# Optimization experiments

Measured on AMD Instinct MI355X. Metric: run time of the kernel, lower is better.

The kernel has to match this reference:

```python
import jax, jax.numpy as jnp
import numpy as np

BS, MA, H, NH = 64, 64, 64, 4  # molecules, max atoms per molecule, hsize, n_heads


def _lengths():
    # deterministic ragged molecule sizes in [24, 64]
    return np.array([24 + (7 * i) % 41 for i in range(BS)], dtype=np.int64)


def _scopes():
    lengths = _lengths()
    N = int(lengths.sum())  # 2774
    scope = np.zeros((BS, MA), dtype=np.int64)      # pad slots gather row 0 (zeros)
    rev = np.zeros((N,), dtype=np.int64)            # flat atom -> b*MA + slot
    pos = 1                                          # flat row 0 is the zero pad row
    for b, L in enumerate(lengths):
        scope[b, :L] = np.arange(pos, pos + L)
        rev[pos - 1:pos - 1 + L] = b * MA + np.arange(L)
        pos += L
    return scope, rev, N


def setup_inputs() -> dict:
    key = jax.random.key(0)
    k0, k1, k2, k3 = jax.random.split(key, 4)
    scope, rev, N = _scopes()
    inputs = jax.random.normal(k0, (N + 1, H), dtype=jnp.float32)
    inputs = inputs.at[0].set(0.0)  # zero pad row, as in graphretro flat tensors
    Wa_pair = jax.random.normal(k1, (H, H * NH), dtype=jnp.float32) * (1.0 / np.sqrt(H))
    Wa_score = jax.random.normal(k2, (H, NH), dtype=jnp.float32) * (1.0 / np.sqrt(H))
    W_proj = jax.random.normal(k3, (H * NH, H), dtype=jnp.float32) * (1.0 / np.sqrt(H * NH))
    return {
        "inputs": inputs,
        "scope_tensor": jnp.asarray(scope),
        "scope_rev_tensor": jnp.asarray(rev),
        "Wa_pair": Wa_pair,
        "Wa_score": Wa_score,
        "W_proj": W_proj,
    }


def reference(inputs, scope_tensor, scope_rev_tensor, Wa_pair, Wa_score, W_proj):
    bs, ma = scope_tensor.shape
    h = inputs.shape[1]
    nh = Wa_score.shape[1]
    # flat_to_batch: [bs, ma, h]; pad slots pull the zero row 0
    c_batch = inputs[scope_tensor]
    # get_pair: pairwise sum of atom embeddings -> [bs, ma, ma, h]
    atom_pair = c_batch[:, :, None, :] + c_batch[:, None, :, :]
    # Wa_pair (no bias) + relu, viewed as [bs, ma, ma, h, nh]
    total_att = jax.nn.relu(atom_pair @ Wa_pair).reshape(bs, ma, ma, h, nh)
    # einsum '...hn,hjn->...jn' with j==1, then sigmoid -> [bs, ma, ma, nh]
    att_score = jax.nn.sigmoid(jnp.einsum('bijhn,hn->bijn', total_att, Wa_score))
    # att_score * c_atom[b,j,h], summed over j -> [bs, ma, h, nh]
    c_sum = jnp.einsum('bijn,bjh->bihn', att_score, c_batch)
    # view to [bs, ma, h*nh] (h-major, matching torch .view) and project
    c_atom_att = c_sum.reshape(bs, ma, h * nh) @ W_proj  # [bs, ma, h]
    c_mol_att = c_atom_att.sum(axis=1)  # [bs, h]
    # batch_to_flat + prepend zero row -> [N+1, h]
    flat = c_atom_att.reshape(bs * ma, h)[scope_rev_tensor]
    c_atom_att_flat = jnp.concatenate([jnp.zeros((1, h), flat.dtype), flat], axis=0)
    return (c_mol_att, c_atom_att_flat)
```

## Files before the change

kernel.cpp:

```cpp
#include <hip/hip_runtime.h>
#include <stdint.h>

typedef _Float16 h2 __attribute__((ext_vector_type(2)));
typedef _Float16 h8 __attribute__((ext_vector_type(8)));
typedef float f32x4 __attribute__((ext_vector_type(4)));
typedef unsigned int u32;
typedef unsigned short u16;

#define WT_STR 68
#define PJ_STR 68
#define WP_STR 268
#define PI_STR 36
#define CB_STR 72
#define CT_STR 68
#define AB_STR 72
#define CS_STR 264
#define WS_STR 36

__device__ __forceinline__ u32 pk2(float a, float b) {
    return __builtin_bit_cast(u32, __builtin_amdgcn_cvt_pkrtz(a, b));
}
__device__ __forceinline__ h8 frag4(u32 a, u32 b, u32 c, u32 d) {
    return __builtin_bit_cast(h8, make_uint4(a, b, c, d));
}

__global__ __launch_bounds__(256, 2) void atom_attn(
    const float* __restrict__ inputs,
    const int*   __restrict__ scope,
    const float* __restrict__ Wa_pair,
    const float* __restrict__ Wa_score,
    const float* __restrict__ W_proj,
    float* __restrict__ out_mol,
    float* __restrict__ out_flat)
{
    __shared__ __align__(16) u16 s_big[256 * WT_STR];
    __shared__ __align__(16) u32 s_pi[4 * 8 * PI_STR];
    __shared__ __align__(16) u16 s_cbcs[64 * CB_STR];
    __shared__ __align__(16) u16 s_ct[64 * CT_STR];
    __shared__ __align__(16) u16 s_ab[32 * AB_STR];
    __shared__ __align__(16) u32 s_ws[4 * WS_STR];

    const int t = threadIdx.x;
    const int w = t >> 6, l = t & 63;
    const int ml = l & 15, q = l >> 4;
    const int b = blockIdx.y, bx = blockIdx.x;
    const int i_base = bx * 8;

    if (t < 128) {
        const int n = t & 3, hh = t >> 2;
        const float g0 = Wa_score[(2 * hh) * 4 + n];
        const float g1 = Wa_score[(2 * hh + 1) * 4 + n];
        s_ws[n * WS_STR + hh] = pk2(g0, g1);
    }
    {
        const int jp = (t & 31) * 2;
        const int pp = t >> 5;
        const int r0 = scope[b * 64 + jp];
        const int r1 = scope[b * 64 + jp + 1];
        const f32x4 a0 = *(const f32x4*)(inputs + (size_t)r0 * 64 + pp * 8);
        const f32x4 a1 = *(const f32x4*)(inputs + (size_t)r0 * 64 + pp * 8 + 4);
        const f32x4 b0 = *(const f32x4*)(inputs + (size_t)r1 * 64 + pp * 8);
        const f32x4 b1 = *(const f32x4*)(inputs + (size_t)r1 * 64 + pp * 8 + 4);
        float A[8] = {a0[0], a0[1], a0[2], a0[3], a1[0], a1[1], a1[2], a1[3]};
        float B[8] = {b0[0], b0[1], b0[2], b0[3], b1[0], b1[1], b1[2], b1[3]};
        *(uint4*)&s_cbcs[jp * CB_STR + pp * 8] =
            make_uint4(pk2(A[0], A[1]), pk2(A[2], A[3]), pk2(A[4], A[5]), pk2(A[6], A[7]));
        *(uint4*)&s_cbcs[(jp + 1) * CB_STR + pp * 8] =
            make_uint4(pk2(B[0], B[1]), pk2(B[2], B[3]), pk2(B[4], B[5]), pk2(B[6], B[7]));
        #pragma unroll
        for (int e = 0; e < 8; ++e)
            *(u32*)&s_ct[(pp * 8 + e) * CT_STR + jp] = pk2(A[e], B[e]);
    }
    {
        const int cg = (t & 127) * 2;
        const int hh2 = t >> 7;
        const int cp0 = (cg & 3) * 64 + (cg >> 2);
        #pragma unroll
        for (int k2 = 0; k2 < 16; ++k2) {
            const int h0 = hh2 * 32 + k2 * 2;
            const float2 r0 = *(const float2*)(Wa_pair + h0 * 256 + cg);
            const float2 r1 = *(const float2*)(Wa_pair + (h0 + 1) * 256 + cg);
            *(u32*)&s_big[cp0 * WT_STR + h0]        = pk2(r0.x, r1.x);
            *(u32*)&s_big[(cp0 + 64) * WT_STR + h0] = pk2(r0.y, r1.y);
        }
    }
    __syncthreads();

    const int mh = w & 1, jp2 = w >> 1;
    f32x4 D[8][2];
    #pragma unroll
    for (int k = 0; k < 8; ++k) { D[k][0] = (f32x4)0.f; D[k][1] = (f32x4)0.f; }
    {
        h8 bf[2][2];
        #pragma unroll
        for (int jt = 0; jt < 2; ++jt)
            #pragma unroll
            for (int ks = 0; ks < 2; ++ks)
                bf[jt][ks] = __builtin_bit_cast(h8,
                    *(const uint4*)&s_cbcs[((jp2 * 2 + jt) * 16 + ml) * CB_STR + ks * 32 + q * 8]);
        #pragma unroll
        for (int k = 0; k < 8; ++k) {
            const int mt = mh * 8 + k;
            #pragma unroll
            for (int ks = 0; ks < 2; ++ks) {
                const uint2 x0 = *(const uint2*)&s_big[(mt * 16 + ml) * WT_STR + ks * 32 + q * 8];
                const uint2 x1 = *(const uint2*)&s_big[(mt * 16 + ml) * WT_STR + ks * 32 + q * 8 + 4];
                const h8 af = frag4(x0.x, x0.y, x1.x, x1.y);
                D[k][0] = __builtin_amdgcn_mfma_f32_16x16x32_f16(af, bf[0][ks], D[k][0], 0, 0, 0);
                D[k][1] = __builtin_amdgcn_mfma_f32_16x16x32_f16(af, bf[1][ks], D[k][1], 0, 0, 0);
            }
        }
    }
    __syncthreads();
    {
        const int wt = bx >> 1, mlo = (bx & 1) * 8;
        #pragma unroll
        for (int k = 0; k < 8; ++k) {
            const int mt = mh * 8 + k;
            const int nb = mt >> 2, h0 = (mt & 3) * 16 + q * 4;
            #pragma unroll
            for (int jt = 0; jt < 2; ++jt) {
                const int jtile = jp2 * 2 + jt;
                const int j = jtile * 16 + ml;
                const u32 p0 = pk2(D[k][jt][0], D[k][jt][1]);
                const u32 p1 = pk2(D[k][jt][2], D[k][jt][3]);
                *(uint2*)&s_big[(nb * 64 + j) * PJ_STR + h0] = make_uint2(p0, p1);
                if (jtile == wt && ml >= mlo && ml < mlo + 8)
                    *(uint2*)&s_pi[(nb * 8 + (ml - mlo)) * PI_STR + (h0 >> 1)] = make_uint2(p0, p1);
            }
        }
    }
    __syncthreads();

    {
        const int n = w;
        u32 pj_u[32];
        #pragma unroll
        for (int k = 0; k < 16; ++k) {
            const uint2 v = *(const uint2*)&s_big[(n * 64 + l) * PJ_STR + k * 4];
            pj_u[2 * k] = v.x; pj_u[2 * k + 1] = v.y;
        }
        u32 ws_u[32];
        #pragma unroll
        for (int k = 0; k < 8; ++k) {
            const uint4 v = *(const uint4*)&s_ws[n * WS_STR + k * 4];
            ws_u[4 * k] = v.x; ws_u[4 * k + 1] = v.y; ws_u[4 * k + 2] = v.z; ws_u[4 * k + 3] = v.w;
        }
        const h2 zero2 = {(_Float16)0.f, (_Float16)0.f};
        #pragma unroll
        for (int ii = 0; ii < 8; ++ii) {
            const u32* pir = &s_pi[(n * 8 + ii) * PI_STR];
            float s0 = 0.f, s1 = 0.f;
            #pragma unroll
            for (int c8 = 0; c8 < 8; ++c8) {
                const uint4 pv = *(const uint4*)&pir[c8 * 4];
                const u32 pe[4] = {pv.x, pv.y, pv.z, pv.w};
                #pragma unroll
                for (int e = 0; e < 4; ++e) {
                    const h2 pi2 = __builtin_bit_cast(h2, pe[e]);
                    const h2 pj2 = __builtin_bit_cast(h2, pj_u[c8 * 4 + e]);
                    h2 tv = pi2 + pj2;
                    tv = __builtin_elementwise_max(tv, zero2);
                    if (e & 1)
                        s1 = __builtin_amdgcn_fdot2(tv,
                                __builtin_bit_cast(h2, ws_u[c8 * 4 + e]), s1, false);
                    else
                        s0 = __builtin_amdgcn_fdot2(tv,
                                __builtin_bit_cast(h2, ws_u[c8 * 4 + e]), s0, false);
                }
            }
            const float s = s0 + s1;
            const float a = 1.f / (1.f + __expf(-s));
            const _Float16 ah = (_Float16)a;
            s_ab[(ii * 4 + n) * AB_STR + l] = __builtin_bit_cast(u16, ah);
        }
    }
    __syncthreads();

    {
        const int o0 = (t & 31) * 2, seg = t >> 5;
        #pragma unroll
        for (int k2 = 0; k2 < 16; ++k2) {
            const int c0 = seg * 32 + k2 * 2;
            const float2 r0 = *(const float2*)(W_proj + c0 * 64 + o0);
            const float2 r1 = *(const float2*)(W_proj + (c0 + 1) * 64 + o0);
            *(u32*)&s_big[o0 * WP_STR + c0]       = pk2(r0.x, r1.x);
            *(u32*)&s_big[(o0 + 1) * WP_STR + c0] = pk2(r0.y, r1.y);
        }
    }
    {
        h8 bfc[2];
        #pragma unroll
        for (int ks = 0; ks < 2; ++ks) {
            const uint2 y0 = *(const uint2*)&s_ct[(w * 16 + ml) * CT_STR + ks * 32 + q * 8];
            const uint2 y1 = *(const uint2*)&s_ct[(w * 16 + ml) * CT_STR + ks * 32 + q * 8 + 4];
            bfc[ks] = frag4(y0.x, y0.y, y1.x, y1.y);
        }
        f32x4 D2[2]; D2[0] = (f32x4)0.f; D2[1] = (f32x4)0.f;
        #pragma unroll
        for (int mt = 0; mt < 2; ++mt)
            #pragma unroll
            for (int ks = 0; ks < 2; ++ks) {
                const h8 af = __builtin_bit_cast(h8,
                    *(const uint4*)&s_ab[(mt * 16 + ml) * AB_STR + ks * 32 + q * 8]);
                D2[mt] = __builtin_amdgcn_mfma_f32_16x16x32_f16(af, bfc[ks], D2[mt], 0, 0, 0);
            }
        #pragma unroll
        for (int mt = 0; mt < 2; ++mt) {
            const int iloc = mt * 4 + q, h = w * 16 + ml;
            *(uint2*)&s_cbcs[iloc * CS_STR + h * 4] =
                make_uint2(pk2(D2[mt][0], D2[mt][1]), pk2(D2[mt][2], D2[mt][3]));
        }
    }
    __syncthreads();

    {
        f32x4 D4 = (f32x4)0.f;
        #pragma unroll
        for (int ks = 0; ks < 8; ++ks) {
            const h8 af = __builtin_bit_cast(h8,
                *(const uint4*)&s_cbcs[ml * CS_STR + ks * 32 + q * 8]);
            const uint2 z0 = *(const uint2*)&s_big[(w * 16 + ml) * WP_STR + ks * 32 + q * 8];
            const uint2 z1 = *(const uint2*)&s_big[(w * 16 + ml) * WP_STR + ks * 32 + q * 8 + 4];
            const h8 bf4 = frag4(z0.x, z0.y, z1.x, z1.y);
            D4 = __builtin_amdgcn_mfma_f32_16x16x32_f16(af, bf4, D4, 0, 0, 0);
        }
        const int o = w * 16 + ml;
        if (q < 2) {
            #pragma unroll
            for (int r = 0; r < 4; ++r) {
                const int iloc = q * 4 + r;
                const int row = scope[b * 64 + i_base + iloc];
                if (row > 0) out_flat[(size_t)row * 64 + o] = D4[r];
            }
        }
        float s4 = (q < 2) ? (D4[0] + D4[1] + D4[2] + D4[3]) : 0.f;
        s4 += __shfl_xor(s4, 16, 64);
        s4 += __shfl_xor(s4, 32, 64);
        if (l < 16) atomicAdd(out_mol + b * 64 + o, s4);
    }
}

extern "C" void kernel_launch(void* const* d_in, const int* in_sizes, int n_in,
                              void* d_out, int out_size, void* d_ws, size_t ws_size,
                              hipStream_t stream) {
    const float* inputs   = (const float*)d_in[0];
    const int*   scope    = (const int*)d_in[1];
    const float* Wa_pair  = (const float*)d_in[3];
    const float* Wa_score = (const float*)d_in[4];
    const float* W_proj   = (const float*)d_in[5];
    float* out = (float*)d_out;

    (void)hipMemsetAsync(d_out, 0, (64 * 64 + 64) * sizeof(float), stream);

    dim3 grid(8, 64);
    atom_attn<<<grid, 256, 0, stream>>>(inputs, scope, Wa_pair, Wa_score,
                                        W_proj, out, out + 64 * 64);
}
```

Measured before the change: 76.00 us.

## Use 512-thread blocks covering 16 atoms each to halve redundant pair-projection work

Each block now handles 16 query atoms instead of 8, using 512 threads and a 4x64 grid. The per-molecule Wa_pair projection of all 64 atoms, which every block recomputes, is therefore done half as often. Shared buffers are split into separate arrays so the W_proj load can run alongside the Wa_pair load and one barrier is removed. The cost is fewer blocks (256 instead of 512), one block per CU with more LDS, and half the waves idle in the final projection step.

```diff
diff --git a/kernel.cpp b/kernel.cpp
--- a/kernel.cpp
+++ b/kernel.cpp
@@ -24,7 +24,7 @@
     return __builtin_bit_cast(h8, make_uint4(a, b, c, d));
 }
 
-__global__ __launch_bounds__(256, 2) void atom_attn(
+__global__ __launch_bounds__(512, 1) void atom_attn(
     const float* __restrict__ inputs,
     const int*   __restrict__ scope,
     const float* __restrict__ Wa_pair,
@@ -33,111 +33,123 @@
     float* __restrict__ out_mol,
     float* __restrict__ out_flat)
 {
-    __shared__ __align__(16) u16 s_big[256 * WT_STR];
-    __shared__ __align__(16) u32 s_pi[4 * 8 * PI_STR];
-    __shared__ __align__(16) u16 s_cbcs[64 * CB_STR];
+    __shared__ __align__(16) u16 s_wa[256 * WT_STR];
+    __shared__ __align__(16) u16 s_pj[256 * PJ_STR];
+    __shared__ __align__(16) u16 s_wp[64 * WP_STR];
+    __shared__ __align__(16) u32 s_pi[4 * 16 * PI_STR];
+    __shared__ __align__(16) u16 s_cb[64 * CB_STR];
     __shared__ __align__(16) u16 s_ct[64 * CT_STR];
-    __shared__ __align__(16) u16 s_ab[32 * AB_STR];
+    __shared__ __align__(16) u16 s_ab[64 * AB_STR];
+    __shared__ __align__(16) u16 s_cs[16 * CS_STR];
     __shared__ __align__(16) u32 s_ws[4 * WS_STR];
 
     const int t = threadIdx.x;
     const int w = t >> 6, l = t & 63;
     const int ml = l & 15, q = l >> 4;
     const int b = blockIdx.y, bx = blockIdx.x;
-    const int i_base = bx * 8;
-
-    if (t < 128) {
-        const int n = t & 3, hh = t >> 2;
-        const float g0 = Wa_score[(2 * hh) * 4 + n];
-        const float g1 = Wa_score[(2 * hh + 1) * 4 + n];
-        s_ws[n * WS_STR + hh] = pk2(g0, g1);
-    }
-    {
-        const int jp = (t & 31) * 2;
-        const int pp = t >> 5;
-        const int r0 = scope[b * 64 + jp];
-        const int r1 = scope[b * 64 + jp + 1];
-        const f32x4 a0 = *(const f32x4*)(inputs + (size_t)r0 * 64 + pp * 8);
-        const f32x4 a1 = *(const f32x4*)(inputs + (size_t)r0 * 64 + pp * 8 + 4);
-        const f32x4 b0 = *(const f32x4*)(inputs + (size_t)r1 * 64 + pp * 8);
-        const f32x4 b1 = *(const f32x4*)(inputs + (size_t)r1 * 64 + pp * 8 + 4);
-        float A[8] = {a0[0], a0[1], a0[2], a0[3], a1[0], a1[1], a1[2], a1[3]};
-        float B[8] = {b0[0], b0[1], b0[2], b0[3], b1[0], b1[1], b1[2], b1[3]};
-        *(uint4*)&s_cbcs[jp * CB_STR + pp * 8] =
-            make_uint4(pk2(A[0], A[1]), pk2(A[2], A[3]), pk2(A[4], A[5]), pk2(A[6], A[7]));
-        *(uint4*)&s_cbcs[(jp + 1) * CB_STR + pp * 8] =
-            make_uint4(pk2(B[0], B[1]), pk2(B[2], B[3]), pk2(B[4], B[5]), pk2(B[6], B[7]));
-        #pragma unroll
-        for (int e = 0; e < 8; ++e)
-            *(u32*)&s_ct[(pp * 8 + e) * CT_STR + jp] = pk2(A[e], B[e]);
-    }
-    {
-        const int cg = (t & 127) * 2;
-        const int hh2 = t >> 7;
+    const int i_base = bx * 16;
+
+    if (t < 256) {
+        if (t < 128) {
+            const int n = t & 3, hh = t >> 2;
+            const float g0 = Wa_score[(2 * hh) * 4 + n];
+            const float g1 = Wa_score[(2 * hh + 1) * 4 + n];
+            s_ws[n * WS_STR + hh] = pk2(g0, g1);
+        }
+        {
+            const int jp = (t & 31) * 2;
+            const int pp = t >> 5;
+            const int r0 = scope[b * 64 + jp];
+            const int r1 = scope[b * 64 + jp + 1];
+            const f32x4 a0 = *(const f32x4*)(inputs + (size_t)r0 * 64 + pp * 8);
+            const f32x4 a1 = *(const f32x4*)(inputs + (size_t)r0 * 64 + pp * 8 + 4);
+            const f32x4 b0 = *(const f32x4*)(inputs + (size_t)r1 * 64 + pp * 8);
+            const f32x4 b1 = *(const f32x4*)(inputs + (size_t)r1 * 64 + pp * 8 + 4);
+            float A[8] = {a0[0], a0[1], a0[2], a0[3], a1[0], a1[1], a1[2], a1[3]};
+            float B[8] = {b0[0], b0[1], b0[2], b0[3], b1[0], b1[1], b1[2], b1[3]};
+            *(uint4*)&s_cb[jp * CB_STR + pp * 8] =
+                make_uint4(pk2(A[0], A[1]), pk2(A[2], A[3]), pk2(A[4], A[5]), pk2(A[6], A[7]));
+            *(uint4*)&s_cb[(jp + 1) * CB_STR + pp * 8] =
+                make_uint4(pk2(B[0], B[1]), pk2(B[2], B[3]), pk2(B[4], B[5]), pk2(B[6], B[7]));
+            #pragma unroll
+            for (int e = 0; e < 8; ++e)
+                *(u32*)&s_ct[(pp * 8 + e) * CT_STR + jp] = pk2(A[e], B[e]);
+        }
+        {
+            const int o0 = (t & 31) * 2, seg = t >> 5;
+            #pragma unroll
+            for (int k2 = 0; k2 < 16; ++k2) {
+                const int c0 = seg * 32 + k2 * 2;
+                const float2 r0 = *(const float2*)(W_proj + c0 * 64 + o0);
+                const float2 r1 = *(const float2*)(W_proj + (c0 + 1) * 64 + o0);
+                *(u32*)&s_wp[o0 * WP_STR + c0]       = pk2(r0.x, r1.x);
+                *(u32*)&s_wp[(o0 + 1) * WP_STR + c0] = pk2(r0.y, r1.y);
+            }
+        }
+    } else {
+        const int t2 = t & 255;
+        const int cg = (t2 & 127) * 2;
+        const int hh2 = t2 >> 7;
         const int cp0 = (cg & 3) * 64 + (cg >> 2);
         #pragma unroll
         for (int k2 = 0; k2 < 16; ++k2) {
             const int h0 = hh2 * 32 + k2 * 2;
             const float2 r0 = *(const float2*)(Wa_pair + h0 * 256 + cg);
             const float2 r1 = *(const float2*)(Wa_pair + (h0 + 1) * 256 + cg);
-            *(u32*)&s_big[cp0 * WT_STR + h0]        = pk2(r0.x, r1.x);
-            *(u32*)&s_big[(cp0 + 64) * WT_STR + h0] = pk2(r0.y, r1.y);
-        }
-    }
-    __syncthreads();
-
-    const int mh = w & 1, jp2 = w >> 1;
-    f32x4 D[8][2];
-    #pragma unroll
-    for (int k = 0; k < 8; ++k) { D[k][0] = (f32x4)0.f; D[k][1] = (f32x4)0.f; }
+            *(u32*)&s_wa[cp0 * WT_STR + h0]        = pk2(r0.x, r1.x);
+            *(u32*)&s_wa[(cp0 + 64) * WT_STR + h0] = pk2(r0.y, r1.y);
+        }
+    }
+    __syncthreads();
+
     {
+        const int mq = w & 3, jh = w >> 2;
+        f32x4 D[4][2];
+        #pragma unroll
+        for (int k = 0; k < 4; ++k) { D[k][0] = (f32x4)0.f; D[k][1] = (f32x4)0.f; }
         h8 bf[2][2];
         #pragma unroll
         for (int jt = 0; jt < 2; ++jt)
             #pragma unroll
             for (int ks = 0; ks < 2; ++ks)
                 bf[jt][ks] = __builtin_bit_cast(h8,
-                    *(const uint4*)&s_cbcs[((jp2 * 2 + jt) * 16 + ml) * CB_STR + ks * 32 + q * 8]);
-        #pragma unroll
-        for (int k = 0; k < 8; ++k) {
-            const int mt = mh * 8 + k;
+                    *(const uint4*)&s_cb[((jh * 2 + jt) * 16 + ml) * CB_STR + ks * 32 + q * 8]);
+        #pragma unroll
+        for (int k = 0; k < 4; ++k) {
+            const int mt = mq * 4 + k;
             #pragma unroll
             for (int ks = 0; ks < 2; ++ks) {
-                const uint2 x0 = *(const uint2*)&s_big[(mt * 16 + ml) * WT_STR + ks * 32 + q * 8];
-                const uint2 x1 = *(const uint2*)&s_big[(mt * 16 + ml) * WT_STR + ks * 32 + q * 8 + 4];
+                const uint2 x0 = *(const uint2*)&s_wa[(mt * 16 + ml) * WT_STR + ks * 32 + q * 8];
+                const uint2 x1 = *(const uint2*)&s_wa[(mt * 16 + ml) * WT_STR + ks * 32 + q * 8 + 4];
                 const h8 af = frag4(x0.x, x0.y, x1.x, x1.y);
                 D[k][0] = __builtin_amdgcn_mfma_f32_16x16x32_f16(af, bf[0][ks], D[k][0], 0, 0, 0);
                 D[k][1] = __builtin_amdgcn_mfma_f32_16x16x32_f16(af, bf[1][ks], D[k][1], 0, 0, 0);
             }
         }
-    }
-    __syncthreads();
-    {
-        const int wt = bx >> 1, mlo = (bx & 1) * 8;
-        #pragma unroll
-        for (int k = 0; k < 8; ++k) {
-            const int mt = mh * 8 + k;
+        #pragma unroll
+        for (int k = 0; k < 4; ++k) {
+            const int mt = mq * 4 + k;
             const int nb = mt >> 2, h0 = (mt & 3) * 16 + q * 4;
             #pragma unroll
             for (int jt = 0; jt < 2; ++jt) {
-                const int jtile = jp2 * 2 + jt;
+                const int jtile = jh * 2 + jt;
                 const int j = jtile * 16 + ml;
                 const u32 p0 = pk2(D[k][jt][0], D[k][jt][1]);
                 const u32 p1 = pk2(D[k][jt][2], D[k][jt][3]);
-                *(uint2*)&s_big[(nb * 64 + j) * PJ_STR + h0] = make_uint2(p0, p1);
-                if (jtile == wt && ml >= mlo && ml < mlo + 8)
-                    *(uint2*)&s_pi[(nb * 8 + (ml - mlo)) * PI_STR + (h0 >> 1)] = make_uint2(p0, p1);
+                *(uint2*)&s_pj[(nb * 64 + j) * PJ_STR + h0] = make_uint2(p0, p1);
+                if (jtile == bx)
+                    *(uint2*)&s_pi[(nb * 16 + ml) * PI_STR + (h0 >> 1)] = make_uint2(p0, p1);
             }
         }
     }
     __syncthreads();
 
     {
-        const int n = w;
+        const int n = w & 3, ih = w >> 2;
         u32 pj_u[32];
         #pragma unroll
         for (int k = 0; k < 16; ++k) {
-            const uint2 v = *(const uint2*)&s_big[(n * 64 + l) * PJ_STR + k * 4];
+            const uint2 v = *(const uint2*)&s_pj[(n * 64 + l) * PJ_STR + k * 4];
             pj_u[2 * k] = v.x; pj_u[2 * k + 1] = v.y;
         }
         u32 ws_u[32];
@@ -149,7 +161,8 @@
         const h2 zero2 = {(_Float16)0.f, (_Float16)0.f};
         #pragma unroll
         for (int ii = 0; ii < 8; ++ii) {
-            const u32* pir = &s_pi[(n * 8 + ii) * PI_STR];
+            const int iloc = ih * 8 + ii;
+            const u32* pir = &s_pi[(n * 16 + iloc) * PI_STR];
             float s0 = 0.f, s1 = 0.f;
             #pragma unroll
             for (int c8 = 0; c8 < 8; ++c8) {
@@ -172,69 +185,55 @@
             const float s = s0 + s1;
             const float a = 1.f / (1.f + __expf(-s));
             const _Float16 ah = (_Float16)a;
-            s_ab[(ii * 4 + n) * AB_STR + l] = __builtin_bit_cast(u16, ah);
+            s_ab[(iloc * 4 + n) * AB_STR + l] = __builtin_bit_cast(u16, ah);
         }
     }
     __syncthreads();
 
     {
-        const int o0 = (t & 31) * 2, seg = t >> 5;
-        #pragma unroll
-        for (int k2 = 0; k2 < 16; ++k2) {
-            const int c0 = seg * 32 + k2 * 2;
-            const float2 r0 = *(const float2*)(W_proj + c0 * 64 + o0);
-            const float2 r1 = *(const float2*)(W_proj + (c0 + 1) * 64 + o0);
-            *(u32*)&s_big[o0 * WP_STR + c0]       = pk2(r0.x, r1.x);
-            *(u32*)&s_big[(o0 + 1) * WP_STR + c0] = pk2(r0.y, r1.y);
-        }
-    }
-    {
-        h8 bfc[2];
-        #pragma unroll
-        for (int ks = 0; ks < 2; ++ks) {
-            const uint2 y0 = *(const uint2*)&s_ct[(w * 16 + ml) * CT_STR + ks * 32 + q * 8];
-            const uint2 y1 = *(const uint2*)&s_ct[(w * 16 + ml) * CT_STR + ks * 32 + q * 8 + 4];
-            bfc[ks] = frag4(y0.x, y0.y, y1.x, y1.y);
-        }
-        f32x4 D2[2]; D2[0] = (f32x4)0.f; D2[1] = (f32x4)0.f;
-        #pragma unroll
-        for (int mt = 0; mt < 2; ++mt)
+        const int mt3 = w & 3, nh = w >> 2;
+        h8 af3[2];
+        #pragma unroll
+        for (int ks = 0; ks < 2; ++ks)
+            af3[ks] = __builtin_bit_cast(h8,
+                *(const uint4*)&s_ab[(mt3 * 16 + ml) * AB_STR + ks * 32 + q * 8]);
+        #pragma unroll
+        for (int nx = 0; nx < 2; ++nx) {
+            const int nt = nh * 2 + nx;
+            f32x4 D2 = (f32x4)0.f;
             #pragma unroll
             for (int ks = 0; ks < 2; ++ks) {
-                const h8 af = __builtin_bit_cast(h8,
-                    *(const uint4*)&s_ab[(mt * 16 + ml) * AB_STR + ks * 32 + q * 8]);
-                D2[mt] = __builtin_amdgcn_mfma_f32_16x16x32_f16(af, bfc[ks], D2[mt], 0, 0, 0);
-            }
-        #pragma unroll
-        for (int mt = 0; mt < 2; ++mt) {
-            const int iloc = mt * 4 + q, h = w * 16 + ml;
-            *(uint2*)&s_cbcs[iloc * CS_STR + h * 4] =
-                make_uint2(pk2(D2[mt][0], D2[mt][1]), pk2(D2[mt][2], D2[mt][3]));
-        }
-    }
-    __syncthreads();
-
-    {
+                const uint2 y0 = *(const uint2*)&s_ct[(nt * 16 + ml) * CT_STR + ks * 32 + q * 8];
+                const uint2 y1 = *(const uint2*)&s_ct[(nt * 16 + ml) * CT_STR + ks * 32 + q * 8 + 4];
+                const h8 bfc = frag4(y0.x, y0.y, y1.x, y1.y);
+                D2 = __builtin_amdgcn_mfma_f32_16x16x32_f16(af3[ks], bfc, D2, 0, 0, 0);
+            }
+            const int iloc = mt3 * 4 + q, h = nt * 16 + ml;
+            *(uint2*)&s_cs[iloc * CS_STR + h * 4] =
+                make_uint2(pk2(D2[0], D2[1]), pk2(D2[2], D2[3]));
+        }
+    }
+    __syncthreads();
+
+    if (w < 4) {
         f32x4 D4 = (f32x4)0.f;
         #pragma unroll
         for (int ks = 0; ks < 8; ++ks) {
             const h8 af = __builtin_bit_cast(h8,
-                *(const uint4*)&s_cbcs[ml * CS_STR + ks * 32 + q * 8]);
-            const uint2 z0 = *(const uint2*)&s_big[(w * 16 + ml) * WP_STR + ks * 32 + q * 8];
-            const uint2 z1 = *(const uint2*)&s_big[(w * 16 + ml) * WP_STR + ks * 32 + q * 8 + 4];
+                *(const uint4*)&s_cs[ml * CS_STR + ks * 32 + q * 8]);
+            const uint2 z0 = *(const uint2*)&s_wp[(w * 16 + ml) * WP_STR + ks * 32 + q * 8];
+            const uint2 z1 = *(const uint2*)&s_wp[(w * 16 + ml) * WP_STR + ks * 32 + q * 8 + 4];
             const h8 bf4 = frag4(z0.x, z0.y, z1.x, z1.y);
             D4 = __builtin_amdgcn_mfma_f32_16x16x32_f16(af, bf4, D4, 0, 0, 0);
         }
         const int o = w * 16 + ml;
-        if (q < 2) {
-            #pragma unroll
-            for (int r = 0; r < 4; ++r) {
-                const int iloc = q * 4 + r;
-                const int row = scope[b * 64 + i_base + iloc];
-                if (row > 0) out_flat[(size_t)row * 64 + o] = D4[r];
-            }
-        }
-        float s4 = (q < 2) ? (D4[0] + D4[1] + D4[2] + D4[3]) : 0.f;
+        #pragma unroll
+        for (int r = 0; r < 4; ++r) {
+            const int iloc = q * 4 + r;
+            const int row = scope[b * 64 + i_base + iloc];
+            if (row > 0) out_flat[(size_t)row * 64 + o] = D4[r];
+        }
+        float s4 = D4[0] + D4[1] + D4[2] + D4[3];
         s4 += __shfl_xor(s4, 16, 64);
         s4 += __shfl_xor(s4, 32, 64);
         if (l < 16) atomicAdd(out_mol + b * 64 + o, s4);
@@ -253,7 +252,7 @@
 
     (void)hipMemsetAsync(d_out, 0, (64 * 64 + 64) * sizeof(float), stream);
 
-    dim3 grid(8, 64);
-    atom_attn<<<grid, 256, 0, stream>>>(inputs, scope, Wa_pair, Wa_score,
+    dim3 grid(4, 64);
+    atom_attn<<<grid, 512, 0, stream>>>(inputs, scope, Wa_pair, Wa_score,
                                         W_proj, out, out + 64 * 64);
 }
```

After: 74.59 us (median of 2 runs). No clear change (-1.8%).
